# Kernel tuning notes

Hardware: AMD Instinct MI355X
Metric: run time of the kernel (lower is better)

## Reference

```python
import jax, jax.numpy as jnp
import numpy as np

B = 262144
N = 256      # mode size of every TT core
R = 8        # tt_rank
D = 8        # number of cores = 7 state dims + 1 action dim
STD = 0.001


def setup_inputs() -> dict:
    key = jax.random.key(0)
    ks = jax.random.split(key, D + 2)
    inp = {}
    # TT cores: G0 (1,N,R), G1..G6 (R,N,R), G7 (R,N,1)
    inp["G0"] = jax.random.normal(ks[0], (1, N, R), dtype=jnp.float32) * STD
    for k in range(1, D - 1):
        inp[f"G{k}"] = jax.random.normal(ks[k], (R, N, R), dtype=jnp.float32) * STD
    inp[f"G{D-1}"] = jax.random.normal(ks[D - 1], (R, N, 1), dtype=jnp.float32) * STD
    inp["states"] = jax.random.randint(ks[D], (B, 7), 0, N, dtype=jnp.int32)
    inp["actions"] = jax.random.randint(ks[D + 1], (B,), 0, N, dtype=jnp.int32)
    return inp


def reference(G0, G1, G2, G3, G4, G5, G6, G7, states, actions):
    # mode 'q_sa': concat state indices with action index -> (B, D)
    idx = jnp.concatenate(
        [states.reshape(-1, 7), actions.reshape(-1, 1)], axis=1
    )
    cores = [G0, G1, G2, G3, G4, G5, G6, G7]
    # t3f.gather_nd: chain of per-core gathers + tiny batched matmuls.
    # vec starts as the gathered slice of the first core: (B, R)
    vec = cores[0][0, idx[:, 0], :]
    for k in range(1, D):
        # gather slices along mode axis: (B, r_prev, r_next)
        sl = jnp.transpose(jnp.take(cores[k], idx[:, k], axis=1), (1, 0, 2))
        vec = jnp.einsum("br,brs->bs", vec, sl)
    # final vec has shape (B, 1); Q(s,a) values per batch element
    return vec[:, 0]
```

## Files before the change

kernel.cpp:

```cpp
#include <hip/hip_runtime.h>


#define NN 256
#define RR 8
#define NR 2048

__device__ __forceinline__ unsigned short f2bf_rne(float f) {
    unsigned int u = __float_as_uint(f);
    u += 0x7FFFu + ((u >> 16) & 1u);
    return (unsigned short)(u >> 16);
}

__global__ __launch_bounds__(256) void transpose_cores(
    const float* __restrict__ G0, const float* __restrict__ G1,
    const float* __restrict__ G2, const float* __restrict__ G3,
    const float* __restrict__ G4, const float* __restrict__ G5,
    const float* __restrict__ G6, const float* __restrict__ G7,
    unsigned short* __restrict__ wsb) {
    const int t = threadIdx.x;
    const int bid = blockIdx.x;

    if (bid < 48) {
        const int k = bid >> 3;
        const int chunk = bid & 7;
        const float* __restrict__ Gk =
            (k == 0) ? G1 : (k == 1) ? G2 : (k == 2) ? G3
          : (k == 3) ? G4 : (k == 4) ? G5 : G6;
        const int n = chunk * 32 + (t >> 3);
        const int r = t & 7;
        const float4* src = (const float4*)(Gk + r * NR + n * RR);
        float4 x = src[0], y = src[1];
        unsigned short* dst = wsb + 2048 + k * 16384 + n * 64 + r * 8;
        unsigned int p0 = f2bf_rne(x.x) | ((unsigned int)f2bf_rne(x.y) << 16);
        unsigned int p1 = f2bf_rne(x.z) | ((unsigned int)f2bf_rne(x.w) << 16);
        unsigned int p2 = f2bf_rne(y.x) | ((unsigned int)f2bf_rne(y.y) << 16);
        unsigned int p3 = f2bf_rne(y.z) | ((unsigned int)f2bf_rne(y.w) << 16);
        *(uint4*)dst = make_uint4(p0, p1, p2, p3);
    } else if (bid == 48) {
        const int n = t;
        const float4* src = (const float4*)(G0 + n * RR);
        float4 x = src[0], y = src[1];
        unsigned short* dst = wsb + n * 8;
        unsigned int p0 = f2bf_rne(x.x) | ((unsigned int)f2bf_rne(x.y) << 16);
        unsigned int p1 = f2bf_rne(x.z) | ((unsigned int)f2bf_rne(x.w) << 16);
        unsigned int p2 = f2bf_rne(y.x) | ((unsigned int)f2bf_rne(y.y) << 16);
        unsigned int p3 = f2bf_rne(y.z) | ((unsigned int)f2bf_rne(y.w) << 16);
        *(uint4*)dst = make_uint4(p0, p1, p2, p3);
    } else {
        const int n = t;
        float f[8];
#pragma unroll
        for (int r = 0; r < 8; ++r) f[r] = G7[r * NN + n];
        unsigned short* dst = wsb + 100352 + n * 8;
        unsigned int p0 = f2bf_rne(f[0]) | ((unsigned int)f2bf_rne(f[1]) << 16);
        unsigned int p1 = f2bf_rne(f[2]) | ((unsigned int)f2bf_rne(f[3]) << 16);
        unsigned int p2 = f2bf_rne(f[4]) | ((unsigned int)f2bf_rne(f[5]) << 16);
        unsigned int p3 = f2bf_rne(f[6]) | ((unsigned int)f2bf_rne(f[7]) << 16);
        *(uint4*)dst = make_uint4(p0, p1, p2, p3);
    }
}

#define BF2F_LO(u) __uint_as_float((u) << 16)
#define BF2F_HI(u) __uint_as_float((u) & 0xFFFF0000u)

#define BSTAGE(koff, nidx)                                                  \
    do {                                                                    \
        const uint4* mp =                                                   \
            (const uint4*)(wsb + 2048 + (koff)*16384 + (nidx)*64);          \
        float nv0 = 0.f, nv1 = 0.f, nv2 = 0.f, nv3 = 0.f;                   \
        float nv4 = 0.f, nv5 = 0.f, nv6 = 0.f, nv7 = 0.f;                   \
        _Pragma("unroll") for (int r = 0; r < 8; ++r) {                     \
            uint4 u = mp[r];                                                \
            float vr = v[r];                                                \
            nv0 += vr * BF2F_LO(u.x); nv1 += vr * BF2F_HI(u.x);             \
            nv2 += vr * BF2F_LO(u.y); nv3 += vr * BF2F_HI(u.y);             \
            nv4 += vr * BF2F_LO(u.z); nv5 += vr * BF2F_HI(u.z);             \
            nv6 += vr * BF2F_LO(u.w); nv7 += vr * BF2F_HI(u.w);             \
        }                                                                   \
        v[0] = nv0; v[1] = nv1; v[2] = nv2; v[3] = nv3;                     \
        v[4] = nv4; v[5] = nv5; v[6] = nv6; v[7] = nv7;                     \
    } while (0)

__global__ __launch_bounds__(256) void tt_gather(
    const unsigned short* __restrict__ wsb,
    const int* __restrict__ states, const int* __restrict__ actions,
    float* __restrict__ out, int B) {
    const int b = blockIdx.x * 256 + threadIdx.x;
    if (b >= B) return;

    const int* srow = states + b * 7;
    const int s0 = srow[0] & 255;
    const int s1 = srow[1] & 255;
    const int s2 = srow[2] & 255;
    const int s3 = srow[3] & 255;
    const int s4 = srow[4] & 255;
    const int s5 = srow[5] & 255;
    const int s6 = srow[6] & 255;
    const int a7 = actions[b] & 255;

    float v[8];
    {
        uint4 u = *(const uint4*)(wsb + s0 * 8);
        v[0] = BF2F_LO(u.x); v[1] = BF2F_HI(u.x);
        v[2] = BF2F_LO(u.y); v[3] = BF2F_HI(u.y);
        v[4] = BF2F_LO(u.z); v[5] = BF2F_HI(u.z);
        v[6] = BF2F_LO(u.w); v[7] = BF2F_HI(u.w);
    }

    BSTAGE(0, s1);
    BSTAGE(1, s2);
    BSTAGE(2, s3);
    BSTAGE(3, s4);
    BSTAGE(4, s5);
    BSTAGE(5, s6);

    float q;
    {
        uint4 u = *(const uint4*)(wsb + 100352 + a7 * 8);
        q = v[0] * BF2F_LO(u.x) + v[1] * BF2F_HI(u.x)
          + v[2] * BF2F_LO(u.y) + v[3] * BF2F_HI(u.y)
          + v[4] * BF2F_LO(u.z) + v[5] * BF2F_HI(u.z)
          + v[6] * BF2F_LO(u.w) + v[7] * BF2F_HI(u.w);
    }
    out[b] = q;
}

extern "C" void kernel_launch(void* const* d_in, const int* in_sizes, int n_in,
                              void* d_out, int out_size, void* d_ws, size_t ws_size,
                              hipStream_t stream) {
    const float* G0 = (const float*)d_in[0];
    const float* G1 = (const float*)d_in[1];
    const float* G2 = (const float*)d_in[2];
    const float* G3 = (const float*)d_in[3];
    const float* G4 = (const float*)d_in[4];
    const float* G5 = (const float*)d_in[5];
    const float* G6 = (const float*)d_in[6];
    const float* G7 = (const float*)d_in[7];
    const int* states  = (const int*)d_in[8];
    const int* actions = (const int*)d_in[9];
    float* out = (float*)d_out;
    int B = in_sizes[9];

    unsigned short* wsb = (unsigned short*)d_ws;

    hipLaunchKernelGGL(transpose_cores, dim3(50), dim3(256), 0, stream,
                       G0, G1, G2, G3, G4, G5, G6, G7, wsb);

    hipLaunchKernelGGL(tt_gather, dim3((B + 255) / 256), dim3(256), 0, stream,
                       wsb, states, actions, out, B);
}
```

Before: 104.0 us.

## Precompute pairwise merged TT cores and stage state indices through shared memory

Folds G0 with G1 into a 256x256x8 table and G6 with G7 into a 256x256x8 table, so each batch element does one fewer gather stage at each end: four stages instead of six. The states array is loaded coalesced into shared memory before each thread reads its own row of indices. The cost is building two 1 MB bf16 tables per call, and random gathers into them will miss cache more often than the old small tables did.

Result: faster. 101.5 us (-2.5%).

```diff
diff --git a/kernel.cpp b/kernel.cpp
--- a/kernel.cpp
+++ b/kernel.cpp
@@ -4,6 +4,8 @@
 #define NN 256
 #define RR 8
 #define NR 2048
+#define U67_OFF 524288
+#define GT_OFF  1048576
 
 __device__ __forceinline__ unsigned short f2bf_rne(float f) {
     unsigned int u = __float_as_uint(f);
@@ -11,7 +13,15 @@
     return (unsigned short)(u >> 16);
 }
 
-__global__ __launch_bounds__(256) void transpose_cores(
+__device__ __forceinline__ uint4 pack8bf(const float* a) {
+    return make_uint4(
+        f2bf_rne(a[0]) | ((unsigned int)f2bf_rne(a[1]) << 16),
+        f2bf_rne(a[2]) | ((unsigned int)f2bf_rne(a[3]) << 16),
+        f2bf_rne(a[4]) | ((unsigned int)f2bf_rne(a[5]) << 16),
+        f2bf_rne(a[6]) | ((unsigned int)f2bf_rne(a[7]) << 16));
+}
+
+__global__ __launch_bounds__(256) void build_tables(
     const float* __restrict__ G0, const float* __restrict__ G1,
     const float* __restrict__ G2, const float* __restrict__ G3,
     const float* __restrict__ G4, const float* __restrict__ G5,
@@ -20,43 +30,47 @@
     const int t = threadIdx.x;
     const int bid = blockIdx.x;
 
-    if (bid < 48) {
-        const int k = bid >> 3;
-        const int chunk = bid & 7;
+    if (bid < NN) {
+        const int n0 = bid, n1 = t;
+        float acc[RR] = {0.f,0.f,0.f,0.f,0.f,0.f,0.f,0.f};
+#pragma unroll
+        for (int r = 0; r < RR; ++r) {
+            float ar = G0[n0 * RR + r];
+            const float4* p = (const float4*)(G1 + r * NR + n1 * RR);
+            float4 x = p[0], y = p[1];
+            acc[0] += ar * x.x; acc[1] += ar * x.y;
+            acc[2] += ar * x.z; acc[3] += ar * x.w;
+            acc[4] += ar * y.x; acc[5] += ar * y.y;
+            acc[6] += ar * y.z; acc[7] += ar * y.w;
+        }
+        *(uint4*)(wsb + n0 * 2048 + n1 * 8) = pack8bf(acc);
+    } else if (bid < 2 * NN) {
+        const int n6 = bid - NN, n7 = t;
+        float g7v[RR];
+#pragma unroll
+        for (int s = 0; s < RR; ++s) g7v[s] = G7[s * NN + n7];
+        float u[RR];
+#pragma unroll
+        for (int r = 0; r < RR; ++r) {
+            float acc = 0.f;
+#pragma unroll
+            for (int s = 0; s < RR; ++s)
+                acc += G6[r * NR + n6 * RR + s] * g7v[s];
+            u[r] = acc;
+        }
+        *(uint4*)(wsb + U67_OFF + n6 * 2048 + n7 * 8) = pack8bf(u);
+    } else {
+        const int q = bid - 2 * NN;
+        const int k = q >> 3;
+        const int chunk = q & 7;
         const float* __restrict__ Gk =
-            (k == 0) ? G1 : (k == 1) ? G2 : (k == 2) ? G3
-          : (k == 3) ? G4 : (k == 4) ? G5 : G6;
+            (k == 0) ? G2 : (k == 1) ? G3 : (k == 2) ? G4 : G5;
         const int n = chunk * 32 + (t >> 3);
         const int r = t & 7;
         const float4* src = (const float4*)(Gk + r * NR + n * RR);
         float4 x = src[0], y = src[1];
-        unsigned short* dst = wsb + 2048 + k * 16384 + n * 64 + r * 8;
-        unsigned int p0 = f2bf_rne(x.x) | ((unsigned int)f2bf_rne(x.y) << 16);
-        unsigned int p1 = f2bf_rne(x.z) | ((unsigned int)f2bf_rne(x.w) << 16);
-        unsigned int p2 = f2bf_rne(y.x) | ((unsigned int)f2bf_rne(y.y) << 16);
-        unsigned int p3 = f2bf_rne(y.z) | ((unsigned int)f2bf_rne(y.w) << 16);
-        *(uint4*)dst = make_uint4(p0, p1, p2, p3);
-    } else if (bid == 48) {
-        const int n = t;
-        const float4* src = (const float4*)(G0 + n * RR);
-        float4 x = src[0], y = src[1];
-        unsigned short* dst = wsb + n * 8;
-        unsigned int p0 = f2bf_rne(x.x) | ((unsigned int)f2bf_rne(x.y) << 16);
-        unsigned int p1 = f2bf_rne(x.z) | ((unsigned int)f2bf_rne(x.w) << 16);
-        unsigned int p2 = f2bf_rne(y.x) | ((unsigned int)f2bf_rne(y.y) << 16);
-        unsigned int p3 = f2bf_rne(y.z) | ((unsigned int)f2bf_rne(y.w) << 16);
-        *(uint4*)dst = make_uint4(p0, p1, p2, p3);
-    } else {
-        const int n = t;
-        float f[8];
-#pragma unroll
-        for (int r = 0; r < 8; ++r) f[r] = G7[r * NN + n];
-        unsigned short* dst = wsb + 100352 + n * 8;
-        unsigned int p0 = f2bf_rne(f[0]) | ((unsigned int)f2bf_rne(f[1]) << 16);
-        unsigned int p1 = f2bf_rne(f[2]) | ((unsigned int)f2bf_rne(f[3]) << 16);
-        unsigned int p2 = f2bf_rne(f[4]) | ((unsigned int)f2bf_rne(f[5]) << 16);
-        unsigned int p3 = f2bf_rne(f[6]) | ((unsigned int)f2bf_rne(f[7]) << 16);
-        *(uint4*)dst = make_uint4(p0, p1, p2, p3);
+        float a[8] = {x.x, x.y, x.z, x.w, y.x, y.y, y.z, y.w};
+        *(uint4*)(wsb + GT_OFF + k * 16384 + n * 64 + r * 8) = pack8bf(a);
     }
 }
 
@@ -66,7 +80,7 @@
 #define BSTAGE(koff, nidx)                                                  \
     do {                                                                    \
         const uint4* mp =                                                   \
-            (const uint4*)(wsb + 2048 + (koff)*16384 + (nidx)*64);          \
+            (const uint4*)(wsb + GT_OFF + (koff)*16384 + (nidx)*64);        \
         float nv0 = 0.f, nv1 = 0.f, nv2 = 0.f, nv3 = 0.f;                   \
         float nv4 = 0.f, nv5 = 0.f, nv6 = 0.f, nv7 = 0.f;                   \
         _Pragma("unroll") for (int r = 0; r < 8; ++r) {                     \
@@ -85,44 +99,56 @@
     const unsigned short* __restrict__ wsb,
     const int* __restrict__ states, const int* __restrict__ actions,
     float* __restrict__ out, int B) {
-    const int b = blockIdx.x * 256 + threadIdx.x;
-    if (b >= B) return;
+    __shared__ int ibuf[NN * 7];
 
-    const int* srow = states + b * 7;
-    const int s0 = srow[0] & 255;
-    const int s1 = srow[1] & 255;
-    const int s2 = srow[2] & 255;
-    const int s3 = srow[3] & 255;
-    const int s4 = srow[4] & 255;
-    const int s5 = srow[5] & 255;
-    const int s6 = srow[6] & 255;
-    const int a7 = actions[b] & 255;
+    const int t = threadIdx.x;
+    const int b = blockIdx.x * 256 + t;
+
+    {
+        const int* gsrc = states + (size_t)blockIdx.x * 256 * 7;
+        const int lim = B * 7 - blockIdx.x * 256 * 7;
+#pragma unroll
+        for (int k = 0; k < 7; ++k) {
+            int j = t + (k << 8);
+            if (j < lim) ibuf[j] = gsrc[j];
+        }
+    }
+    __syncthreads();
+
+    const bool active = (b < B);
+    const int* row = ibuf + t * 7;
+    const int s0 = row[0] & 255;
+    const int s1 = row[1] & 255;
+    const int s2 = row[2] & 255;
+    const int s3 = row[3] & 255;
+    const int s4 = row[4] & 255;
+    const int s5 = row[5] & 255;
+    const int s6 = row[6] & 255;
+    const int a7 = actions[active ? b : 0] & 255;
 
     float v[8];
     {
-        uint4 u = *(const uint4*)(wsb + s0 * 8);
+        uint4 u = *(const uint4*)(wsb + s0 * 2048 + s1 * 8);
         v[0] = BF2F_LO(u.x); v[1] = BF2F_HI(u.x);
         v[2] = BF2F_LO(u.y); v[3] = BF2F_HI(u.y);
         v[4] = BF2F_LO(u.z); v[5] = BF2F_HI(u.z);
         v[6] = BF2F_LO(u.w); v[7] = BF2F_HI(u.w);
     }
 
-    BSTAGE(0, s1);
-    BSTAGE(1, s2);
-    BSTAGE(2, s3);
-    BSTAGE(3, s4);
-    BSTAGE(4, s5);
-    BSTAGE(5, s6);
+    BSTAGE(0, s2);
+    BSTAGE(1, s3);
+    BSTAGE(2, s4);
+    BSTAGE(3, s5);
 
     float q;
     {
-        uint4 u = *(const uint4*)(wsb + 100352 + a7 * 8);
+        uint4 u = *(const uint4*)(wsb + U67_OFF + s6 * 2048 + a7 * 8);
         q = v[0] * BF2F_LO(u.x) + v[1] * BF2F_HI(u.x)
           + v[2] * BF2F_LO(u.y) + v[3] * BF2F_HI(u.y)
           + v[4] * BF2F_LO(u.z) + v[5] * BF2F_HI(u.z)
           + v[6] * BF2F_LO(u.w) + v[7] * BF2F_HI(u.w);
     }
-    out[b] = q;
+    if (active) out[b] = q;
 }
 
 extern "C" void kernel_launch(void* const* d_in, const int* in_sizes, int n_in,
@@ -143,7 +169,7 @@
 
     unsigned short* wsb = (unsigned short*)d_ws;
 
-    hipLaunchKernelGGL(transpose_cores, dim3(50), dim3(256), 0, stream,
+    hipLaunchKernelGGL(build_tables, dim3(2 * NN + 32), dim3(256), 0, stream,
                        G0, G1, G2, G3, G4, G5, G6, G7, wsb);
 
     hipLaunchKernelGGL(tt_gather, dim3((B + 255) / 256), dim3(256), 0, stream,
```
